# Kernel optimization log

Measured on AMD Instinct MI355X. Metric: run time of the kernel, lower is better.

Reference implementation:

```python
import jax, jax.numpy as jnp
import numpy as np

B, T, E, H = 2, 2048, 1024, 16
HS = E // H  # head size 64


def setup_inputs() -> dict:
    key = jax.random.key(0)
    ks = jax.random.split(key, 6)
    s = 0.02
    return {
        "x": jax.random.normal(ks[0], (B, T, E), dtype=jnp.float32),
        "Wq": jax.random.normal(ks[1], (E, E), dtype=jnp.float32) * s,
        "Wk": jax.random.normal(ks[2], (E, E), dtype=jnp.float32) * s,
        "Wv": jax.random.normal(ks[3], (E, E), dtype=jnp.float32) * s,
        "Wp": jax.random.normal(ks[4], (E, E), dtype=jnp.float32) * s,
        "bp": jax.random.normal(ks[5], (E,), dtype=jnp.float32) * s,
    }


def reference(x, Wq, Wk, Wv, Wp, bp):
    b, t, e = x.shape
    # per-head projections (concatenated heads == single E->E matmul, reshaped)
    def heads(w):
        return jnp.einsum('bte,ef->btf', x, w).reshape(b, t, H, HS).transpose(0, 2, 1, 3)
    q, k, v = heads(Wq), heads(Wk), heads(Wv)  # [B,H,T,HS]
    # NOTE: original scales by full embed dim E, not head_size
    scores = jnp.einsum('bhqd,bhkd->bhqk', q, k) * (e ** -0.5)
    causal = jnp.tril(jnp.ones((t, t), dtype=bool))
    scores = jnp.where(causal, scores, -jnp.inf)
    probs = jax.nn.softmax(scores, axis=-1)
    # dropout is identity in eval mode
    out = jnp.einsum('bhqk,bhkd->bhqd', probs, v)  # [B,H,T,HS]
    out = out.transpose(0, 2, 1, 3).reshape(b, t, e)
    return jnp.einsum('bte,ef->btf', out, Wp) + bp
```

## Files before the change

### kernel.cpp

```cpp
#include <hip/hip_runtime.h>
#include <math.h>

typedef __bf16 bf16x8 __attribute__((ext_vector_type(8)));
typedef __bf16 bf16x4 __attribute__((ext_vector_type(4)));
typedef float f32x4 __attribute__((ext_vector_type(4)));

constexpr int Bb = 2, Tt = 2048, Ee = 1024, Hh = 16, Hs = 64;
constexpr int Mm = Bb * Tt;

__device__ inline unsigned short f2bf(float f) {
    union { float f; unsigned u; } c; c.f = f;
    unsigned u = c.u;
    u += 0x7FFFu + ((u >> 16) & 1u);
    return (unsigned short)(u >> 16);
}

__device__ inline void gl2lds16(const void* g, void* l) {
    __builtin_amdgcn_global_load_lds(
        (const __attribute__((address_space(1))) void*)g,
        (__attribute__((address_space(3))) void*)l, 16, 0, 0);
}

__global__ __launch_bounds__(256) void prep(const float* __restrict__ x,
                                            const float* __restrict__ Wq,
                                            const float* __restrict__ Wk,
                                            const float* __restrict__ Wv,
                                            const float* __restrict__ Wp,
                                            unsigned short* __restrict__ xb,
                                            unsigned short* __restrict__ wt3,
                                            unsigned short* __restrict__ wpt) {
    const int tid = threadIdx.x;
    if (blockIdx.z == 4) {
        int flat = (blockIdx.y * 16 + blockIdx.x) * 256 + tid;
#pragma unroll
        for (int i = 0; i < 16; i++) {
            int gid = flat + i * 65536;
            float4 v = ((const float4*)x)[gid];
            ushort4 o;
            o.x = f2bf(v.x); o.y = f2bf(v.y); o.z = f2bf(v.z); o.w = f2bf(v.w);
            ((ushort4*)xb)[gid] = o;
        }
        return;
    }
    __shared__ unsigned short t[64][68];
    const float* W = (blockIdx.z == 0) ? Wq : (blockIdx.z == 1) ? Wk
                    : (blockIdx.z == 2) ? Wv : Wp;
    unsigned short* dst = (blockIdx.z < 3) ? wt3 + (size_t)blockIdx.z * 1024 * 1024 : wpt;
    const int k0 = blockIdx.x * 64, n0 = blockIdx.y * 64;
#pragma unroll
    for (int j = 0; j < 4; j++) {
        int row = (tid >> 4) + j * 16;
        int c4 = (tid & 15) * 4;
        float4 v = *(const float4*)&W[(size_t)(k0 + row) * 1024 + n0 + c4];
        t[row][c4 + 0] = f2bf(v.x); t[row][c4 + 1] = f2bf(v.y);
        t[row][c4 + 2] = f2bf(v.z); t[row][c4 + 3] = f2bf(v.w);
    }
    __syncthreads();
#pragma unroll
    for (int j = 0; j < 16; j++) {
        int flat = j * 256 + tid;
        int orow = flat >> 6, ocol = flat & 63;
        dst[(size_t)(n0 + orow) * 1024 + k0 + ocol] = t[ocol][orow];
    }
}

__device__ inline void gemm_mainloop(const unsigned short* __restrict__ A,
                                     const unsigned short* __restrict__ Bt,
                                     unsigned short* As, unsigned short* Bs,
                                     int bm, int bn, int tid, f32x4 (&acc)[4][4]) {
    const int lane = tid & 63, w = tid >> 6;
    const int quad = lane >> 4, cl = lane & 15;
    const int wm = (w >> 1) * 64, wn = (w & 1) * 64;

    auto stage = [&](int k0) {
#pragma unroll
        for (int i = 0; i < 2; i++) {
            int L = tid + i * 256;
            int r = L >> 2;
            int kc = (L & 3) ^ (r & 3);
            gl2lds16(A + (size_t)(bm + r) * 1024 + k0 + kc * 8, &As[L * 8]);
        }
#pragma unroll
        for (int i = 0; i < 2; i++) {
            int L = tid + i * 256;
            int r = L >> 2;
            int kc = (L & 3) ^ (r & 3);
            gl2lds16(Bt + (size_t)(bn + r) * 1024 + k0 + kc * 8, &Bs[L * 8]);
        }
    };

    stage(0);
    __syncthreads();
    for (int k0 = 0;;) {
        bf16x8 af[4], bfr[4];
#pragma unroll
        for (int mt = 0; mt < 4; mt++) {
            int r = wm + mt * 16 + cl;
            af[mt] = *(const bf16x8*)&As[(r * 4 + (quad ^ (r & 3))) * 8];
            int rb = wn + mt * 16 + cl;
            bfr[mt] = *(const bf16x8*)&Bs[(rb * 4 + (quad ^ (rb & 3))) * 8];
        }
#pragma unroll
        for (int mt = 0; mt < 4; mt++)
#pragma unroll
            for (int nt = 0; nt < 4; nt++)
                acc[mt][nt] = __builtin_amdgcn_mfma_f32_16x16x32_bf16(
                    af[mt], bfr[nt], acc[mt][nt], 0, 0, 0);
        k0 += 32;
        if (k0 >= 1024) break;
        __syncthreads();
        stage(k0);
        __syncthreads();
    }
}

__global__ __launch_bounds__(256, 2) void gemm_qkv(const unsigned short* __restrict__ A,
                                                   const unsigned short* __restrict__ Bt,
                                                   unsigned short* __restrict__ qb,
                                                   unsigned short* __restrict__ kb,
                                                   unsigned short* __restrict__ vtb) {
    __shared__ unsigned short As[128 * 32];
    __shared__ unsigned short Bs[128 * 32];
    const int tid = threadIdx.x;
    const int bm = blockIdx.y * 128;
    const int bn = blockIdx.x * 128;
    f32x4 acc[4][4] = {};
    gemm_mainloop(A, Bt, As, Bs, bm, bn, tid, acc);

    const int lane = tid & 63, w = tid >> 6;
    const int quad = lane >> 4, cl = lane & 15;
    const int wm = (w >> 1) * 64, wn = (w & 1) * 64;
    const int region = bn >> 10;

    if (region < 2) {
        unsigned short* dst = region ? kb : qb;
        const float qs = region ? 1.0f : 0.045084220027780107f;
#pragma unroll
        for (int mt = 0; mt < 4; mt++)
#pragma unroll
            for (int nt = 0; nt < 4; nt++)
#pragma unroll
                for (int rg = 0; rg < 4; rg++) {
                    int m = bm + wm + mt * 16 + quad * 4 + rg;
                    int nn = (bn + wn + nt * 16 + cl) & 1023;
                    int b = m >> 11, t = m & 2047, h = nn >> 6, hs = nn & 63;
                    dst[((size_t)(b * 16 + h) * 2048 + t) * 64 + hs] =
                        f2bf(acc[mt][nt][rg] * qs);
                }
    } else {
#pragma unroll
        for (int mt = 0; mt < 4; mt++) {
            int m0 = bm + wm + mt * 16 + quad * 4;
            int b = m0 >> 11, t0 = m0 & 2047;
#pragma unroll
            for (int nt = 0; nt < 4; nt++) {
                int nn = (bn + wn + nt * 16 + cl) & 1023;
                int h = nn >> 6, hs = nn & 63;
                ushort4 pk;
                pk.x = f2bf(acc[mt][nt][0]); pk.y = f2bf(acc[mt][nt][1]);
                pk.z = f2bf(acc[mt][nt][2]); pk.w = f2bf(acc[mt][nt][3]);
                *(ushort4*)&vtb[((size_t)(b * 16 + h) * 64 + hs) * 2048 + t0] = pk;
            }
        }
    }
}

__global__ __launch_bounds__(256, 4) void gemm_out(const unsigned short* __restrict__ A,
                                                   const unsigned short* __restrict__ Bt,
                                                   const float* __restrict__ bias,
                                                   float* __restrict__ out) {
    __shared__ unsigned short As[64 * 32];
    __shared__ unsigned short Bs[128 * 32];
    const int tid = threadIdx.x;
    const int bm = blockIdx.y * 64;
    const int bn = blockIdx.x * 128;
    const int lane = tid & 63, w = tid >> 6;
    const int quad = lane >> 4, cl = lane & 15;
    const int wm = (w >> 1) * 32, wn = (w & 1) * 64;
    f32x4 acc[2][4] = {};

    auto stage = [&](int k0) {
        {
            int L = tid;
            int r = L >> 2;
            int kc = (L & 3) ^ (r & 3);
            gl2lds16(A + (size_t)(bm + r) * 1024 + k0 + kc * 8, &As[L * 8]);
        }
#pragma unroll
        for (int i = 0; i < 2; i++) {
            int L = tid + i * 256;
            int r = L >> 2;
            int kc = (L & 3) ^ (r & 3);
            gl2lds16(Bt + (size_t)(bn + r) * 1024 + k0 + kc * 8, &Bs[L * 8]);
        }
    };

    stage(0);
    __syncthreads();
    for (int k0 = 0;;) {
        bf16x8 af[2], bfr[4];
#pragma unroll
        for (int mt = 0; mt < 2; mt++) {
            int r = wm + mt * 16 + cl;
            af[mt] = *(const bf16x8*)&As[(r * 4 + (quad ^ (r & 3))) * 8];
        }
#pragma unroll
        for (int nt = 0; nt < 4; nt++) {
            int rb = wn + nt * 16 + cl;
            bfr[nt] = *(const bf16x8*)&Bs[(rb * 4 + (quad ^ (rb & 3))) * 8];
        }
#pragma unroll
        for (int mt = 0; mt < 2; mt++)
#pragma unroll
            for (int nt = 0; nt < 4; nt++)
                acc[mt][nt] = __builtin_amdgcn_mfma_f32_16x16x32_bf16(
                    af[mt], bfr[nt], acc[mt][nt], 0, 0, 0);
        k0 += 32;
        if (k0 >= 1024) break;
        __syncthreads();
        stage(k0);
        __syncthreads();
    }

#pragma unroll
    for (int mt = 0; mt < 2; mt++)
#pragma unroll
        for (int nt = 0; nt < 4; nt++)
#pragma unroll
            for (int rg = 0; rg < 4; rg++) {
                int m = bm + wm + mt * 16 + quad * 4 + rg;
                int n = bn + wn + nt * 16 + cl;
                out[(size_t)m * 1024 + n] = acc[mt][nt][rg] + bias[n];
            }
}

__global__ __launch_bounds__(256, 3) void attn_mfma(const unsigned short* __restrict__ qg,
                                                    const unsigned short* __restrict__ kg,
                                                    const unsigned short* __restrict__ vtg,
                                                    unsigned short* __restrict__ og) {
    __shared__ unsigned short lds[24576];
    unsigned short* Plds = lds;
    float* Cmb = (float*)(lds + 8192);
    float* Ll  = (float*)(lds + 22528);

    const int tid = threadIdx.x;
    const int idx = blockIdx.x;
    const int bh = idx & 31;
    const int qt = 31 - (idx >> 5);
    const int lane = tid & 63, w = tid >> 6;
    const int quad = lane >> 4, cl = lane & 15;
    const int p = w >> 1;
    const int qhalf = w & 1;
    const int qbase = qt * 64;
    const unsigned short* qB = qg + (size_t)bh * 2048 * 64;
    const unsigned short* kB = kg + (size_t)bh * 2048 * 64;
    const unsigned short* vB = vtg + (size_t)bh * 64 * 2048;

    auto stageKV = [&](int kt, int buf) {
        unsigned short* Kd = lds + 8192 + buf * 8192;
        unsigned short* Vd = lds + 12288 + buf * 8192;
#pragma unroll
        for (int i = 0; i < 2; i++) {
            int L = tid + i * 256;
            int r = L >> 3;
            int kc = (L & 7) ^ (r & 7);
            gl2lds16(kB + (size_t)(kt * 64 + r) * 64 + kc * 8, &Kd[L * 8]);
            gl2lds16(vB + (size_t)r * 2048 + kt * 64 + kc * 8, &Vd[L * 8]);
        }
    };

    bf16x8 qf[2][2];
#pragma unroll
    for (int nt2 = 0; nt2 < 2; nt2++)
#pragma unroll
        for (int kf = 0; kf < 2; kf++) {
            int row = qbase + qhalf * 32 + nt2 * 16 + cl;
            qf[nt2][kf] = *(const bf16x8*)&qB[(size_t)row * 64 + (kf * 4 + quad) * 8];
        }

    bf16x8 ones;
#pragma unroll
    for (int i = 0; i < 8; i++) ones[i] = (__bf16)1.0f;

    f32x4 oacc[2][4] = {};
    f32x4 lacc[2] = {};
    unsigned short* Pw = &Plds[w * 2048];
    const unsigned short* Kl = lds + 8192 + p * 8192;
    const unsigned short* Vl = lds + 12288 + p * 8192;
    const int nit = (qt + 2) >> 1;

    for (int i = 0; i < nit; i++) {
        stageKV(2 * i, 0);
        if (2 * i + 1 <= qt) stageKV(2 * i + 1, 1);
        __syncthreads();

        const int kt = 2 * i + p;
        if (kt <= qt) {
            const bool diag = (kt == qt);
            f32x4 sac[4][2] = {};
#pragma unroll
            for (int kf = 0; kf < 2; kf++)
#pragma unroll
                for (int mt = 0; mt < 4; mt++) {
                    int r = mt * 16 + cl, cc = kf * 4 + quad;
                    bf16x8 kf8 = *(const bf16x8*)&Kl[(r * 8 + (cc ^ (r & 7))) * 8];
#pragma unroll
                    for (int nt2 = 0; nt2 < 2; nt2++)
                        sac[mt][nt2] = __builtin_amdgcn_mfma_f32_16x16x32_bf16(
                            kf8, qf[nt2][kf], sac[mt][nt2], 0, 0, 0);
                }
#pragma unroll
            for (int mt = 0; mt < 4; mt++)
#pragma unroll
                for (int nt2 = 0; nt2 < 2; nt2++) {
                    bf16x4 p4;
#pragma unroll
                    for (int rg = 0; rg < 4; rg++) {
                        float pv = exp2f(sac[mt][nt2][rg]);
                        if (diag && (mt * 16 + quad * 4 + rg > nt2 * 16 + cl + qhalf * 32))
                            pv = 0.0f;
                        p4[rg] = (__bf16)pv;
                    }
                    int r2 = nt2 * 16 + cl;
                    int c = mt * 2 + (quad >> 1);
                    *(bf16x4*)&Pw[(r2 * 8 + (c ^ (r2 & 7))) * 8 + (quad & 1) * 4] = p4;
                }
#pragma unroll
            for (int ks = 0; ks < 2; ks++) {
                bf16x8 pf[2];
#pragma unroll
                for (int mt2 = 0; mt2 < 2; mt2++) {
                    int r2 = mt2 * 16 + cl, cc = ks * 4 + quad;
                    pf[mt2] = *(const bf16x8*)&Pw[(r2 * 8 + (cc ^ (r2 & 7))) * 8];
                }
#pragma unroll
                for (int mt2 = 0; mt2 < 2; mt2++)
                    lacc[mt2] = __builtin_amdgcn_mfma_f32_16x16x32_bf16(
                        pf[mt2], ones, lacc[mt2], 0, 0, 0);
#pragma unroll
                for (int nt = 0; nt < 4; nt++) {
                    int r = nt * 16 + cl, cc = ks * 4 + quad;
                    bf16x8 vf = *(const bf16x8*)&Vl[(r * 8 + (cc ^ (r & 7))) * 8];
#pragma unroll
                    for (int mt2 = 0; mt2 < 2; mt2++)
                        oacc[mt2][nt] = __builtin_amdgcn_mfma_f32_16x16x32_bf16(
                            pf[mt2], vf, oacc[mt2][nt], 0, 0, 0);
                }
            }
        }
        __syncthreads();
    }

    if (p == 1) {
#pragma unroll
        for (int mt2 = 0; mt2 < 2; mt2++)
#pragma unroll
            for (int rg = 0; rg < 4; rg++) {
                int row = qhalf * 32 + mt2 * 16 + quad * 4 + rg;
                if (cl == 0) Ll[row] = lacc[mt2][rg];
#pragma unroll
                for (int nt = 0; nt < 4; nt++)
                    Cmb[row * 68 + nt * 16 + cl] = oacc[mt2][nt][rg];
            }
    }
    __syncthreads();
    if (p == 0) {
        const int b = bh >> 4, h = bh & 15;
#pragma unroll
        for (int mt2 = 0; mt2 < 2; mt2++)
#pragma unroll
            for (int rg = 0; rg < 4; rg++) {
                int row = qhalf * 32 + mt2 * 16 + quad * 4 + rg;
                float inv = 1.0f / (lacc[mt2][rg] + Ll[row]);
                int t = qbase + row;
#pragma unroll
                for (int nt = 0; nt < 4; nt++) {
                    int hs = nt * 16 + cl;
                    float val = oacc[mt2][nt][rg] + Cmb[row * 68 + nt * 16 + cl];
                    og[((size_t)(b * 2048 + t)) * 1024 + h * 64 + hs] = f2bf(val * inv);
                }
            }
    }
}

extern "C" void kernel_launch(void* const* d_in, const int* in_sizes, int n_in,
                              void* d_out, int out_size, void* d_ws, size_t ws_size,
                              hipStream_t stream) {
    const float* x = (const float*)d_in[0];
    const float* Wq = (const float*)d_in[1];
    const float* Wk = (const float*)d_in[2];
    const float* Wv = (const float*)d_in[3];
    const float* Wp = (const float*)d_in[4];
    const float* bp = (const float*)d_in[5];
    float* out = (float*)d_out;

    unsigned short* xb = (unsigned short*)d_ws;
    unsigned short* wt3 = xb + (size_t)Mm * Ee;
    unsigned short* wpt = wt3 + (size_t)3 * Ee * Ee;
    unsigned short* qb = wpt + (size_t)Ee * Ee;
    unsigned short* kb = qb + (size_t)Mm * Ee;
    unsigned short* vtb = kb + (size_t)Mm * Ee;
    unsigned short* ab = vtb + (size_t)Mm * Ee;

    prep<<<dim3(16, 16, 5), dim3(256), 0, stream>>>(x, Wq, Wk, Wv, Wp, xb, wt3, wpt);
    gemm_qkv<<<dim3(24, 32), dim3(256), 0, stream>>>(xb, wt3, qb, kb, vtb);
    attn_mfma<<<dim3(1024), dim3(256), 0, stream>>>(qb, kb, vtb, ab);
    gemm_out<<<dim3(8, 64), dim3(256), 0, stream>>>(ab, wpt, bp, out);
}
```

Before: 173.8 us.

## Shrink attention LDS footprint, halve P buffer, raise occupancy to 4 blocks

The per-wave P staging buffer is halved by converting and consuming probabilities one 32-key slice at a time. The LDS layout is reorganised so K/V buffers come first and the combine scratch aliases them, cutting shared memory from 48KB to 40KB. The launch bound rises from 3 to 4 blocks per CU. A cheaper pack-to-bf16 via perm with round-half-up replaces the per-element conversion. This lowers the register budget, which risks spills, and the rounding differs slightly from round-to-nearest-even.

```diff
diff --git a/kernel.cpp b/kernel.cpp
--- a/kernel.cpp
+++ b/kernel.cpp
@@ -19,6 +19,12 @@
     __builtin_amdgcn_global_load_lds(
         (const __attribute__((address_space(1))) void*)g,
         (__attribute__((address_space(3))) void*)l, 16, 0, 0);
+}
+
+__device__ inline unsigned pk_bf16(float a, float b) {
+    union { float f; unsigned u; } ca, cb;
+    ca.f = a; cb.f = b;
+    return __builtin_amdgcn_perm(ca.u + 0x8000u, cb.u + 0x8000u, 0x07060302u);
 }
 
 __global__ __launch_bounds__(256) void prep(const float* __restrict__ x,
@@ -234,14 +240,13 @@
             }
 }
 
-__global__ __launch_bounds__(256, 3) void attn_mfma(const unsigned short* __restrict__ qg,
+__global__ __launch_bounds__(256, 4) void attn_mfma(const unsigned short* __restrict__ qg,
                                                     const unsigned short* __restrict__ kg,
                                                     const unsigned short* __restrict__ vtg,
                                                     unsigned short* __restrict__ og) {
-    __shared__ unsigned short lds[24576];
-    unsigned short* Plds = lds;
-    float* Cmb = (float*)(lds + 8192);
-    float* Ll  = (float*)(lds + 22528);
+    __shared__ unsigned short lds[20480];
+    float* Cmb = (float*)lds;
+    float* Ll = (float*)(lds + 8704);
 
     const int tid = threadIdx.x;
     const int idx = blockIdx.x;
@@ -257,8 +262,8 @@
     const unsigned short* vB = vtg + (size_t)bh * 64 * 2048;
 
     auto stageKV = [&](int kt, int buf) {
-        unsigned short* Kd = lds + 8192 + buf * 8192;
-        unsigned short* Vd = lds + 12288 + buf * 8192;
+        unsigned short* Kd = lds + buf * 8192;
+        unsigned short* Vd = lds + 4096 + buf * 8192;
 #pragma unroll
         for (int i = 0; i < 2; i++) {
             int L = tid + i * 256;
@@ -284,9 +289,9 @@
 
     f32x4 oacc[2][4] = {};
     f32x4 lacc[2] = {};
-    unsigned short* Pw = &Plds[w * 2048];
-    const unsigned short* Kl = lds + 8192 + p * 8192;
-    const unsigned short* Vl = lds + 12288 + p * 8192;
+    unsigned short* Pw = lds + 16384 + w * 1024;
+    const unsigned short* Kl = lds + p * 8192;
+    const unsigned short* Vl = lds + 4096 + p * 8192;
     const int nit = (qt + 2) >> 1;
 
     for (int i = 0; i < nit; i++) {
@@ -310,28 +315,34 @@
                             kf8, qf[nt2][kf], sac[mt][nt2], 0, 0, 0);
                 }
 #pragma unroll
-            for (int mt = 0; mt < 4; mt++)
-#pragma unroll
-                for (int nt2 = 0; nt2 < 2; nt2++) {
-                    bf16x4 p4;
-#pragma unroll
-                    for (int rg = 0; rg < 4; rg++) {
-                        float pv = exp2f(sac[mt][nt2][rg]);
-                        if (diag && (mt * 16 + quad * 4 + rg > nt2 * 16 + cl + qhalf * 32))
-                            pv = 0.0f;
-                        p4[rg] = (__bf16)pv;
+            for (int ks = 0; ks < 2; ks++) {
+#pragma unroll
+                for (int mtl = 0; mtl < 2; mtl++)
+#pragma unroll
+                    for (int nt2 = 0; nt2 < 2; nt2++) {
+                        float pv[4];
+#pragma unroll
+                        for (int rg = 0; rg < 4; rg++) {
+                            float e = exp2f(sac[ks * 2 + mtl][nt2][rg]);
+                            if (diag && (ks * 32 + mtl * 16 + quad * 4 + rg >
+                                         nt2 * 16 + cl + qhalf * 32))
+                                e = 0.0f;
+                            pv[rg] = e;
+                        }
+                        uint2 d;
+                        d.x = pk_bf16(pv[1], pv[0]);
+                        d.y = pk_bf16(pv[3], pv[2]);
+                        int r2 = nt2 * 16 + cl;
+                        int c = mtl * 2 + (quad >> 1);
+                        int pc = c ^ ((r2 >> 1) & 3);
+                        *(uint2*)&Pw[r2 * 32 + pc * 8 + (quad & 1) * 4] = d;
                     }
-                    int r2 = nt2 * 16 + cl;
-                    int c = mt * 2 + (quad >> 1);
-                    *(bf16x4*)&Pw[(r2 * 8 + (c ^ (r2 & 7))) * 8 + (quad & 1) * 4] = p4;
-                }
-#pragma unroll
-            for (int ks = 0; ks < 2; ks++) {
                 bf16x8 pf[2];
 #pragma unroll
                 for (int mt2 = 0; mt2 < 2; mt2++) {
-                    int r2 = mt2 * 16 + cl, cc = ks * 4 + quad;
-                    pf[mt2] = *(const bf16x8*)&Pw[(r2 * 8 + (cc ^ (r2 & 7))) * 8];
+                    int r2 = mt2 * 16 + cl;
+                    int pc = quad ^ ((r2 >> 1) & 3);
+                    pf[mt2] = *(const bf16x8*)&Pw[r2 * 32 + pc * 8];
                 }
 #pragma unroll
                 for (int mt2 = 0; mt2 < 2; mt2++)
```

New measurement: 175.7 us. About the same (+1.0%).
